# Kernel tuning notes

Hardware: AMD Instinct MI355X
Metric: run time of the kernel (lower is better)

Reference implementation:

```python
import jax, jax.numpy as jnp
import numpy as np

B, I, H = 4096, 2048, 2048


def setup_inputs() -> dict:
    key = jax.random.key(0)
    k1, k2, k3, k4, k5 = jax.random.split(key, 5)
    return {
        "x": jax.random.normal(k1, (B, I), dtype=jnp.float32),
        "coefficients": jax.random.normal(k2, (I, H), dtype=jnp.float32) * 0.1,
        "amplitude_an": jax.random.normal(k3, (1, I, H), dtype=jnp.float32) * 0.1,
        "amplitude_bn": jax.random.normal(k4, (1, I, H), dtype=jnp.float32) * 0.1,
        "bias": jax.random.normal(k5, (1, I), dtype=jnp.float32),
    }


def reference(x, coefficients, amplitude_an, amplitude_bn, bias):
    # phase[b,h] = x[b,:] @ coefficients[:,h]  (same matmul done per-sample in torch loop)
    phase = x @ coefficients  # [B, H]
    num_harmonics = coefficients.shape[1]
    # sum over harmonics of an[i,h]*cos(phase[b,h]) + bn[i,h]*sin(phase[b,h])
    gain = (
        jnp.einsum("bh,ih->bi", jnp.cos(phase), amplitude_an[0])
        + jnp.einsum("bh,ih->bi", jnp.sin(phase), amplitude_bn[0])
        + num_harmonics * bias  # bias added per-harmonic before the sum over H
    )
    return gain  # [B, I]
```

## Files before the change

kernel.cpp:

```cpp
#include <hip/hip_runtime.h>
#include <hip/hip_bf16.h>

#define B_DIM 4096
#define I_DIM 2048
#define H_DIM 2048

typedef unsigned char u8;
typedef unsigned short u16;
typedef unsigned int u32;
typedef __attribute__((ext_vector_type(4))) float f32x4;
typedef __attribute__((ext_vector_type(4))) int i32x4;
typedef __attribute__((ext_vector_type(8))) int i32x8;

__device__ __forceinline__ void gload_lds16(const void* g, void* l) {
  __builtin_amdgcn_global_load_lds(
      (const __attribute__((address_space(1))) void*)g,
      (__attribute__((address_space(3))) void*)l, 16, 0, 0);
}

__device__ __forceinline__ u32 f2fp4(float v, float inv_scale) {
  const float a = fabsf(v) * inv_scale;
  u32 m = (u32)(a > 0.25f) + (u32)(a > 0.75f) + (u32)(a > 1.25f) +
          (u32)(a > 1.75f) + (u32)(a > 2.5f) + (u32)(a > 3.5f) + (u32)(a > 5.0f);
  return ((__float_as_uint(v) >> 31) << 3) | m;
}

__global__ void prep_all(const float* __restrict__ x, const float* __restrict__ coeff,
                         const float* __restrict__ an, const float* __restrict__ bn,
                         u16* __restrict__ xf4, u16* __restrict__ ct4,
                         u32* __restrict__ ab4) {
  if (blockIdx.x < 4096) {
    __shared__ float tile[32][33];
    const int h0 = (blockIdx.x & 63) * 32;
    const int i0 = (blockIdx.x >> 6) * 32;
    const int tid = threadIdx.x;
    const int tx = tid & 31;
    const int ty = tid >> 5;
    for (int r = ty; r < 32; r += 8)
      tile[r][tx] = coeff[(long)(i0 + r) * H_DIM + (h0 + tx)];
    __syncthreads();
    const int hl = tid >> 3;
    const int q = (tid & 7) * 4;
    u32 w = f2fp4(tile[q + 0][hl], 8.f) | (f2fp4(tile[q + 1][hl], 8.f) << 4) |
            (f2fp4(tile[q + 2][hl], 8.f) << 8) | (f2fp4(tile[q + 3][hl], 8.f) << 12);
    ct4[(long)(h0 + hl) * (I_DIM / 4) + ((i0 + q) >> 2)] = (u16)w;
    return;
  }
  const long NX4 = (long)B_DIM * I_DIM / 4;
  const long NA4 = (long)I_DIM * H_DIM / 4;
  const long total = NX4 + NA4;
  const long stride = (long)1024 * blockDim.x;
  for (long t = (long)(blockIdx.x - 4096) * blockDim.x + threadIdx.x; t < total;
       t += stride) {
    if (t < NX4) {
      float4 v = *(const float4*)(x + t * 4);
      u32 b0 = f2fp4(v.x, 1.f) | (f2fp4(v.y, 1.f) << 4);
      u32 b1 = f2fp4(v.z, 1.f) | (f2fp4(v.w, 1.f) << 4);
      xf4[t] = (u16)(b0 | (b1 << 8));
    } else {
      long p = (t - NX4) * 4;
      float4 va = *(const float4*)(an + p);
      float4 vb = *(const float4*)(bn + p);
      u32 b0 = f2fp4(va.x, 8.f) | (f2fp4(vb.x, 8.f) << 4);
      u32 b1 = f2fp4(va.y, 8.f) | (f2fp4(vb.y, 8.f) << 4);
      u32 b2 = f2fp4(va.z, 8.f) | (f2fp4(vb.z, 8.f) << 4);
      u32 b3 = f2fp4(va.w, 8.f) | (f2fp4(vb.w, 8.f) << 4);
      ab4[p >> 2] = b0 | (b1 << 8) | (b2 << 16) | (b3 << 24);
    }
  }
}

__device__ __forceinline__ void stage_tile(const char* Ab, const char* Bb, long kbyte,
                                           long lda, long ldb, char* AsB, char* BsB,
                                           int tid) {
#pragma unroll
  for (int i = 0; i < 4; ++i) {
    const int o = i * 4096 + tid * 16;
    const int row = o >> 7;
    const int ls = ((((o >> 4) & 7) ^ (row & 7)) << 4);
    gload_lds16(Ab + (long)row * lda + kbyte + ls, AsB + o);
  }
#pragma unroll
  for (int i = 0; i < 4; ++i) {
    const int o = i * 4096 + tid * 16;
    const int row = o >> 7;
    const int ls = ((((o >> 4) & 7) ^ (row & 7)) << 4);
    gload_lds16(Bb + (long)row * ldb + kbyte + ls, BsB + o);
  }
}

__device__ __forceinline__ i32x4 frag_ld16(const char* S, int row, int slot) {
  return *(const i32x4*)(S + row * 128 + ((slot ^ (row & 7)) << 4));
}

template <int SA, int SB>
__device__ __forceinline__ void gemm_kloop_fp4(const char* __restrict__ A,
                                               const char* __restrict__ Bt,
                                               int rowA0, int colB0, long Kbytes,
                                               char* smem, f32x4 acc[4][4]) {
  const int tid = threadIdx.x;
  const int lane = tid & 63;
  const int wid = tid >> 6;
  const int wr = wid >> 1, wc = wid & 1;
  const long lda = Kbytes, ldb = Kbytes;
  const char* Ab = A + (long)rowA0 * lda;
  const char* Bb = Bt + (long)colB0 * ldb;
  const int arow = wr * 64 + (lane & 15);
  const int brow = wc * 64 + (lane & 15);
  const int g = lane >> 4;
  const int nt = (int)(Kbytes >> 7);
  char* AsB = smem;
  char* BsB = smem + 16384;

  stage_tile(Ab, Bb, 0, lda, ldb, AsB, BsB, tid);
  stage_tile(Ab, Bb, 128, lda, ldb, AsB + 32768, BsB + 32768, tid);

  for (int t = 0; t < nt; ++t) {
    const int cur = (t & 1) << 15;
    if (t < nt - 1) asm volatile("s_waitcnt vmcnt(8)" ::: "memory");
    else            asm volatile("s_waitcnt vmcnt(0)" ::: "memory");
    __builtin_amdgcn_sched_barrier(0);
    __builtin_amdgcn_s_barrier();
    __builtin_amdgcn_sched_barrier(0);

    i32x8 af[8], bfr[8];
#pragma unroll
    for (int s = 0; s < 2; ++s)
#pragma unroll
      for (int m = 0; m < 4; ++m) {
        *(i32x4*)&af[s * 4 + m]  = frag_ld16(AsB + cur, arow + m * 16, s * 4 + g);
        *(i32x4*)&bfr[s * 4 + m] = frag_ld16(BsB + cur, brow + m * 16, s * 4 + g);
      }
    asm volatile("s_waitcnt lgkmcnt(0)" ::: "memory");
    __builtin_amdgcn_sched_barrier(0);
    __builtin_amdgcn_s_barrier();
    __builtin_amdgcn_sched_barrier(0);

    if (t + 2 < nt)
      stage_tile(Ab, Bb, (long)(t + 2) * 128, lda, ldb, AsB + cur, BsB + cur, tid);

    __builtin_amdgcn_s_setprio(1);
#pragma unroll
    for (int s = 0; s < 2; ++s)
#pragma unroll
      for (int m = 0; m < 4; ++m)
#pragma unroll
        for (int n = 0; n < 4; ++n)
          acc[m][n] = __builtin_amdgcn_mfma_scale_f32_16x16x128_f8f6f4(
              af[s * 4 + m], bfr[s * 4 + n], acc[m][n], 4, 4, 0, SA, 0, SB);
    __builtin_amdgcn_s_setprio(0);
    __builtin_amdgcn_sched_barrier(0);
  }
}

__device__ __forceinline__ void tile_xy(int& bx, int& by) {
  const int bid = blockIdx.x;
  const int xcd = bid & 7;
  const int loc = bid >> 3;
  const int cy = xcd >> 1;
  const int cx = xcd & 1;
  by = cy * 8 + (loc >> 3);
  bx = cx * 8 + (loc & 7);
}

__global__ __launch_bounds__(256) void gemm_phase(const char* __restrict__ xf4,
                                                  const char* __restrict__ ct4,
                                                  u8* __restrict__ cs4) {
  __shared__ __align__(16) char smem[65536];
  int bx, by;
  tile_xy(bx, by);
  const int rowA0 = by * 128;
  const int colB0 = bx * 128;
  f32x4 acc[4][4];
#pragma unroll
  for (int m = 0; m < 4; ++m)
#pragma unroll
    for (int n = 0; n < 4; ++n)
#pragma unroll
      for (int j = 0; j < 4; ++j) acc[m][n][j] = 0.0f;

  gemm_kloop_fp4<0x7F7F7F7F, 0x7C7C7C7C>(xf4, ct4, rowA0, colB0, I_DIM / 2, smem, acc);

  const int lane = threadIdx.x & 63;
  const int wid = threadIdx.x >> 6;
  const int wr = wid >> 1, wc = wid & 1;
#pragma unroll
  for (int m = 0; m < 4; ++m) {
#pragma unroll
    for (int n = 0; n < 4; ++n) {
      const int col = colB0 + wc * 64 + n * 16 + (lane & 15);
#pragma unroll
      for (int j = 0; j < 4; ++j) {
        const int row = rowA0 + wr * 64 + m * 16 + (lane >> 4) * 4 + j;
        const float p = acc[m][n][j];
        const u32 b = f2fp4(__cosf(p), 4.f) | (f2fp4(__sinf(p), 4.f) << 4);
        cs4[(long)row * H_DIM + col] = (u8)b;
      }
    }
  }
}

__global__ __launch_bounds__(256) void gemm_gain(const char* __restrict__ cs4,
                                                 const char* __restrict__ ab4,
                                                 const float* __restrict__ bias,
                                                 float* __restrict__ out) {
  __shared__ __align__(16) char smem[65536];
  int bx, by;
  tile_xy(bx, by);
  const int rowA0 = by * 128;
  const int colB0 = bx * 128;
  f32x4 acc[4][4];
#pragma unroll
  for (int m = 0; m < 4; ++m)
#pragma unroll
    for (int n = 0; n < 4; ++n)
#pragma unroll
      for (int j = 0; j < 4; ++j) acc[m][n][j] = 0.0f;

  gemm_kloop_fp4<0x7D7D7D7D, 0x7C7C7C7C>(cs4, ab4, rowA0, colB0, H_DIM, smem, acc);

  const int lane = threadIdx.x & 63;
  const int wid = threadIdx.x >> 6;
  const int wr = wid >> 1, wc = wid & 1;
#pragma unroll
  for (int m = 0; m < 4; ++m) {
#pragma unroll
    for (int n = 0; n < 4; ++n) {
      const int col = colB0 + wc * 64 + n * 16 + (lane & 15);
      const float bv = 2048.0f * bias[col];
#pragma unroll
      for (int j = 0; j < 4; ++j) {
        const int row = rowA0 + wr * 64 + m * 16 + (lane >> 4) * 4 + j;
        out[(long)row * I_DIM + col] = acc[m][n][j] + bv;
      }
    }
  }
}

extern "C" void kernel_launch(void* const* d_in, const int* in_sizes, int n_in,
                              void* d_out, int out_size, void* d_ws, size_t ws_size,
                              hipStream_t stream) {
  const float* x     = (const float*)d_in[0];
  const float* coeff = (const float*)d_in[1];
  const float* an    = (const float*)d_in[2];
  const float* bn    = (const float*)d_in[3];
  const float* bias  = (const float*)d_in[4];
  float* out = (float*)d_out;

  char* ws = (char*)d_ws;
  char* xf4 = ws;
  char* ct4 = ws + (4L << 20);
  char* ab4 = ws + (8L << 20);
  u8*  cs4  = (u8*)(ws + (12L << 20));

  prep_all<<<5120, 256, 0, stream>>>(x, coeff, an, bn, (u16*)xf4, (u16*)ct4,
                                     (u32*)ab4);
  gemm_phase<<<512, 256, 0, stream>>>(xf4, ct4, cs4);
  gemm_gain<<<512, 256, 0, stream>>>((const char*)cs4, (const char*)ab4, bias, out);
}
```

Measured before the change: 66.16 us.

## Overlap an/bn quantization with phase GEMM and use triple-buffered 64-byte K tiles

The an/bn FP4 packing moves out of the prep kernel into extra blocks of the phase GEMM launch, so that memory-bound conversion can run alongside the compute-bound GEMM. The phase GEMM also switches to a 64-byte K-step with three rotating LDS buffers and a smaller shared-memory footprint, which may allow more resident blocks per CU. In exchange it issues twice as many barriers and loop iterations, and the conversion blocks compete with the GEMM blocks for CU slots.

```diff
diff --git a/kernel.cpp b/kernel.cpp
--- a/kernel.cpp
+++ b/kernel.cpp
@@ -12,6 +12,8 @@
 typedef __attribute__((ext_vector_type(4))) int i32x4;
 typedef __attribute__((ext_vector_type(8))) int i32x8;
 
+#define SBAR __builtin_amdgcn_sched_barrier(0)
+
 __device__ __forceinline__ void gload_lds16(const void* g, void* l) {
   __builtin_amdgcn_global_load_lds(
       (const __attribute__((address_space(1))) void*)g,
@@ -25,10 +27,8 @@
   return ((__float_as_uint(v) >> 31) << 3) | m;
 }
 
-__global__ void prep_all(const float* __restrict__ x, const float* __restrict__ coeff,
-                         const float* __restrict__ an, const float* __restrict__ bn,
-                         u16* __restrict__ xf4, u16* __restrict__ ct4,
-                         u32* __restrict__ ab4) {
+__global__ void prep_xc(const float* __restrict__ x, const float* __restrict__ coeff,
+                        u16* __restrict__ xf4, u16* __restrict__ ct4) {
   if (blockIdx.x < 4096) {
     __shared__ float tile[32][33];
     const int h0 = (blockIdx.x & 63) * 32;
@@ -47,25 +47,163 @@
     return;
   }
   const long NX4 = (long)B_DIM * I_DIM / 4;
-  const long NA4 = (long)I_DIM * H_DIM / 4;
-  const long total = NX4 + NA4;
-  const long stride = (long)1024 * blockDim.x;
-  for (long t = (long)(blockIdx.x - 4096) * blockDim.x + threadIdx.x; t < total;
+  const long stride = (long)512 * blockDim.x;
+  for (long t = (long)(blockIdx.x - 4096) * blockDim.x + threadIdx.x; t < NX4;
        t += stride) {
-    if (t < NX4) {
-      float4 v = *(const float4*)(x + t * 4);
-      u32 b0 = f2fp4(v.x, 1.f) | (f2fp4(v.y, 1.f) << 4);
-      u32 b1 = f2fp4(v.z, 1.f) | (f2fp4(v.w, 1.f) << 4);
-      xf4[t] = (u16)(b0 | (b1 << 8));
-    } else {
-      long p = (t - NX4) * 4;
+    float4 v = *(const float4*)(x + t * 4);
+    u32 b0 = f2fp4(v.x, 1.f) | (f2fp4(v.y, 1.f) << 4);
+    u32 b1 = f2fp4(v.z, 1.f) | (f2fp4(v.w, 1.f) << 4);
+    xf4[t] = (u16)(b0 | (b1 << 8));
+  }
+}
+
+__device__ __forceinline__ void tile_xy(int& bx, int& by) {
+  const int bid = blockIdx.x;
+  const int xcd = bid & 7;
+  const int loc = bid >> 3;
+  const int cy = xcd >> 1;
+  const int cx = xcd & 1;
+  by = cy * 8 + (loc >> 3);
+  bx = cx * 8 + (loc & 7);
+}
+
+__device__ __forceinline__ void stage64(const char* Ab, const char* Bb, long kbyte,
+                                        long lda, long ldb, char* buf, int tid) {
+#pragma unroll
+  for (int i = 0; i < 2; ++i) {
+    const int o = i * 4096 + tid * 16;
+    const int row = o >> 6;
+    const int ls = ((((o >> 4) & 3) ^ ((row >> 1) & 3)) << 4);
+    gload_lds16(Ab + (long)row * lda + kbyte + ls, buf + o);
+  }
+#pragma unroll
+  for (int i = 0; i < 2; ++i) {
+    const int o = i * 4096 + tid * 16;
+    const int row = o >> 6;
+    const int ls = ((((o >> 4) & 3) ^ ((row >> 1) & 3)) << 4);
+    gload_lds16(Bb + (long)row * ldb + kbyte + ls, buf + 8192 + o);
+  }
+}
+
+__device__ __forceinline__ i32x4 frag_ld64(const char* S, int row, int slot) {
+  return *(const i32x4*)(S + row * 64 + ((slot ^ ((row >> 1) & 3)) << 4));
+}
+
+template <int SA, int SB>
+__device__ __forceinline__ void gemm_kloop64(const char* __restrict__ A,
+                                             const char* __restrict__ Bt,
+                                             int rowA0, int colB0, long Kbytes,
+                                             char* smem, f32x4 acc[4][4]) {
+  const int tid = threadIdx.x;
+  const int lane = tid & 63;
+  const int wid = tid >> 6;
+  const int wr = wid >> 1, wc = wid & 1;
+  const long lda = Kbytes, ldb = Kbytes;
+  const char* Ab = A + (long)rowA0 * lda;
+  const char* Bb = Bt + (long)colB0 * ldb;
+  const int arow = wr * 64 + (lane & 15);
+  const int brow = wc * 64 + (lane & 15);
+  const int g = lane >> 4;
+  const int nt = (int)(Kbytes >> 6);
+
+  char* b0 = smem;
+  char* b1 = smem + 16384;
+  char* b2 = smem + 32768;
+
+  stage64(Ab, Bb, 0, lda, ldb, b0, tid);
+  stage64(Ab, Bb, 64, lda, ldb, b1, tid);
+
+  for (int t = 0; t < nt; ++t) {
+    if (t < nt - 1) asm volatile("s_waitcnt vmcnt(4)" ::: "memory");
+    else            asm volatile("s_waitcnt vmcnt(0)" ::: "memory");
+    SBAR;
+    __builtin_amdgcn_s_barrier();
+    SBAR;
+
+    i32x4 af[4], bfr[4];
+#pragma unroll
+    for (int m = 0; m < 4; ++m) {
+      af[m]  = frag_ld64(b0, arow + m * 16, g);
+      bfr[m] = frag_ld64(b0 + 8192, brow + m * 16, g);
+    }
+    asm volatile("s_waitcnt lgkmcnt(0)" ::: "memory");
+    SBAR;
+    __builtin_amdgcn_s_barrier();
+    SBAR;
+
+    if (t + 2 < nt)
+      stage64(Ab, Bb, (long)(t + 2) * 64, lda, ldb, b2, tid);
+    SBAR;
+
+    i32x8 a8[4], b8[4];
+#pragma unroll
+    for (int m = 0; m < 4; ++m) { *(i32x4*)&a8[m] = af[m]; *(i32x4*)&b8[m] = bfr[m]; }
+    __builtin_amdgcn_s_setprio(1);
+#pragma unroll
+    for (int m = 0; m < 4; ++m)
+#pragma unroll
+      for (int n = 0; n < 4; ++n)
+        acc[m][n] = __builtin_amdgcn_mfma_scale_f32_16x16x128_f8f6f4(
+            a8[m], b8[n], acc[m][n], 4, 4, 0, SA, 0, SB);
+    __builtin_amdgcn_s_setprio(0);
+    SBAR;
+
+    char* tmp = b0; b0 = b1; b1 = b2; b2 = tmp;
+  }
+}
+
+__global__ __launch_bounds__(256) void phase_ab(const char* __restrict__ xf4,
+                                                const char* __restrict__ ct4,
+                                                u8* __restrict__ cs4,
+                                                const float* __restrict__ an,
+                                                const float* __restrict__ bn,
+                                                u32* __restrict__ ab4) {
+  __shared__ __align__(16) char smem[49152];
+  if (blockIdx.x >= 512) {
+    const long NA4 = (long)I_DIM * H_DIM / 4;
+    const long stride = (long)256 * blockDim.x;
+    for (long t = (long)(blockIdx.x - 512) * blockDim.x + threadIdx.x; t < NA4;
+         t += stride) {
+      long p = t * 4;
       float4 va = *(const float4*)(an + p);
       float4 vb = *(const float4*)(bn + p);
       u32 b0 = f2fp4(va.x, 8.f) | (f2fp4(vb.x, 8.f) << 4);
       u32 b1 = f2fp4(va.y, 8.f) | (f2fp4(vb.y, 8.f) << 4);
       u32 b2 = f2fp4(va.z, 8.f) | (f2fp4(vb.z, 8.f) << 4);
       u32 b3 = f2fp4(va.w, 8.f) | (f2fp4(vb.w, 8.f) << 4);
-      ab4[p >> 2] = b0 | (b1 << 8) | (b2 << 16) | (b3 << 24);
+      ab4[t] = b0 | (b1 << 8) | (b2 << 16) | (b3 << 24);
+    }
+    return;
+  }
+  int bx, by;
+  tile_xy(bx, by);
+  const int rowA0 = by * 128;
+  const int colB0 = bx * 128;
+  f32x4 acc[4][4];
+#pragma unroll
+  for (int m = 0; m < 4; ++m)
+#pragma unroll
+    for (int n = 0; n < 4; ++n)
+#pragma unroll
+      for (int j = 0; j < 4; ++j) acc[m][n][j] = 0.0f;
+
+  gemm_kloop64<0x7F7F7F7F, 0x7C7C7C7C>(xf4, ct4, rowA0, colB0, I_DIM / 2, smem, acc);
+
+  const int lane = threadIdx.x & 63;
+  const int wid = threadIdx.x >> 6;
+  const int wr = wid >> 1, wc = wid & 1;
+#pragma unroll
+  for (int m = 0; m < 4; ++m) {
+#pragma unroll
+    for (int n = 0; n < 4; ++n) {
+      const int col = colB0 + wc * 64 + n * 16 + (lane & 15);
+#pragma unroll
+      for (int j = 0; j < 4; ++j) {
+        const int row = rowA0 + wr * 64 + m * 16 + (lane >> 4) * 4 + j;
+        const float p = acc[m][n][j];
+        const u32 b = f2fp4(__cosf(p), 4.f) | (f2fp4(__sinf(p), 4.f) << 4);
+        cs4[(long)row * H_DIM + col] = (u8)b;
+      }
     }
   }
 }
@@ -119,9 +257,9 @@
     const int cur = (t & 1) << 15;
     if (t < nt - 1) asm volatile("s_waitcnt vmcnt(8)" ::: "memory");
     else            asm volatile("s_waitcnt vmcnt(0)" ::: "memory");
-    __builtin_amdgcn_sched_barrier(0);
+    SBAR;
     __builtin_amdgcn_s_barrier();
-    __builtin_amdgcn_sched_barrier(0);
+    SBAR;
 
     i32x8 af[8], bfr[8];
 #pragma unroll
@@ -132,9 +270,9 @@
         *(i32x4*)&bfr[s * 4 + m] = frag_ld16(BsB + cur, brow + m * 16, s * 4 + g);
       }
     asm volatile("s_waitcnt lgkmcnt(0)" ::: "memory");
-    __builtin_amdgcn_sched_barrier(0);
+    SBAR;
     __builtin_amdgcn_s_barrier();
-    __builtin_amdgcn_sched_barrier(0);
+    SBAR;
 
     if (t + 2 < nt)
       stage_tile(Ab, Bb, (long)(t + 2) * 128, lda, ldb, AsB + cur, BsB + cur, tid);
@@ -149,54 +287,7 @@
           acc[m][n] = __builtin_amdgcn_mfma_scale_f32_16x16x128_f8f6f4(
               af[s * 4 + m], bfr[s * 4 + n], acc[m][n], 4, 4, 0, SA, 0, SB);
     __builtin_amdgcn_s_setprio(0);
-    __builtin_amdgcn_sched_barrier(0);
-  }
-}
-
-__device__ __forceinline__ void tile_xy(int& bx, int& by) {
-  const int bid = blockIdx.x;
-  const int xcd = bid & 7;
-  const int loc = bid >> 3;
-  const int cy = xcd >> 1;
-  const int cx = xcd & 1;
-  by = cy * 8 + (loc >> 3);
-  bx = cx * 8 + (loc & 7);
-}
-
-__global__ __launch_bounds__(256) void gemm_phase(const char* __restrict__ xf4,
-                                                  const char* __restrict__ ct4,
-                                                  u8* __restrict__ cs4) {
-  __shared__ __align__(16) char smem[65536];
-  int bx, by;
-  tile_xy(bx, by);
-  const int rowA0 = by * 128;
-  const int colB0 = bx * 128;
-  f32x4 acc[4][4];
-#pragma unroll
-  for (int m = 0; m < 4; ++m)
-#pragma unroll
-    for (int n = 0; n < 4; ++n)
-#pragma unroll
-      for (int j = 0; j < 4; ++j) acc[m][n][j] = 0.0f;
-
-  gemm_kloop_fp4<0x7F7F7F7F, 0x7C7C7C7C>(xf4, ct4, rowA0, colB0, I_DIM / 2, smem, acc);
-
-  const int lane = threadIdx.x & 63;
-  const int wid = threadIdx.x >> 6;
-  const int wr = wid >> 1, wc = wid & 1;
-#pragma unroll
-  for (int m = 0; m < 4; ++m) {
-#pragma unroll
-    for (int n = 0; n < 4; ++n) {
-      const int col = colB0 + wc * 64 + n * 16 + (lane & 15);
-#pragma unroll
-      for (int j = 0; j < 4; ++j) {
-        const int row = rowA0 + wr * 64 + m * 16 + (lane >> 4) * 4 + j;
-        const float p = acc[m][n][j];
-        const u32 b = f2fp4(__cosf(p), 4.f) | (f2fp4(__sinf(p), 4.f) << 4);
-        cs4[(long)row * H_DIM + col] = (u8)b;
-      }
-    }
+    SBAR;
   }
 }
 
@@ -253,8 +344,7 @@
   char* ab4 = ws + (8L << 20);
   u8*  cs4  = (u8*)(ws + (12L << 20));
 
-  prep_all<<<5120, 256, 0, stream>>>(x, coeff, an, bn, (u16*)xf4, (u16*)ct4,
-                                     (u32*)ab4);
-  gemm_phase<<<512, 256, 0, stream>>>(xf4, ct4, cs4);
+  prep_xc<<<4608, 256, 0, stream>>>(x, coeff, (u16*)xf4, (u16*)ct4);
+  phase_ab<<<768, 256, 0, stream>>>(xf4, ct4, cs4, an, bn, (u32*)ab4);
   gemm_gain<<<512, 256, 0, stream>>>((const char*)cs4, (const char*)ab4, bias, out);
 }
```

After: 68.10 us. +2.9%, slower.
